# Performance work log

Measured on AMD Instinct MI355X. Metric: run time of the kernel, lower is better.

Reference implementation:

```python
import jax, jax.numpy as jnp
import numpy as np


def _inside_quad(pts9, quads):
    """Ray-casting point-in-polygon test (semantics of the pointsJf CUDA kernel),
    evaluated only for matched (diagonal) point/box pairs.

    pts9:  [N, 9, 2] points
    quads: [N, 8] polygon corners (x1,y1,x2,y2,x3,y3,x4,y4)
    returns inside flag [N, 9] float32 in {0.0, 1.0}
    """
    vx = quads[:, 0::2][:, None, :]          # [N,1,4]
    vy = quads[:, 1::2][:, None, :]          # [N,1,4]
    vxj = jnp.roll(vx, 1, axis=-1)           # previous vertex (j = i-1 mod 4)
    vyj = jnp.roll(vy, 1, axis=-1)
    px = pts9[..., 0:1]                      # [N,9,1]
    py = pts9[..., 1:2]                      # [N,9,1]
    straddles = (vy > py) != (vyj > py)      # edge crosses horizontal ray
    # x coordinate of edge at height py (only meaningful where straddles)
    x_int = (vxj - vx) * (py - vy) / (vyj - vy) + vx
    crossings = straddles & (px < x_int)     # [N,9,4] bool
    inside = (jnp.sum(crossings.astype(jnp.int32), axis=-1) % 2)
    return inside.astype(jnp.float32)        # [N,9]


def _spatial_border_loss(pts, gt_bboxes, weight, loss_weight):
    n = pts.shape[0]
    pts9 = pts.reshape(n, 9, 2)
    inside = _inside_quad(pts9, gt_bboxes)                    # [N,9]
    out_mask = (inside == 0.0).astype(pts.dtype)              # points outside their gt box
    cx = (gt_bboxes[:, 0] + gt_bboxes[:, 4]) * 0.5
    cy = (gt_bboxes[:, 1] + gt_bboxes[:, 5]) * 0.5
    center = jnp.stack([cx, cy], axis=1)[:, None, :]          # [N,1,2]
    dist = 0.2 * jnp.sqrt(jnp.sum((pts9 - center) ** 2, axis=-1))  # [N,9]
    cnt = jnp.sum(out_mask)
    loss_sb = jnp.where(cnt > 0, jnp.sum(dist * out_mask) / jnp.maximum(cnt, 1.0), 0.0)
    # weighted_spatial_border_loss: avg_factor = sum(weight_repeated4 > 0)/4 + 1e-6
    avg_factor = jnp.sum((weight > 0).astype(jnp.float32)) + 1e-6
    return loss_weight * (loss_sb / avg_factor)[None]          # shape [1]


def setup_inputs() -> dict:
    key = jax.random.key(0)
    k1, k2, k3 = jax.random.split(key, 3)
    N = 1_000_000
    pts = jax.random.normal(k1, (N, 18), dtype=jnp.float32)
    gt_bboxes = jax.random.normal(k2, (N, 8), dtype=jnp.float32)
    weight = jax.random.uniform(k3, (N,), dtype=jnp.float32)
    return {"pts": pts, "gt_bboxes": gt_bboxes, "weight": weight}


def reference(pts, gt_bboxes, weight):
    return _spatial_border_loss(pts, gt_bboxes, weight, loss_weight=1.0)
```

## Files before the change

kernel.cpp:

```cpp
#include <hip/hip_runtime.h>


#define SBL_NBLOCKS 2048
#define SBL_BLOCK   256

__global__ void __launch_bounds__(SBL_BLOCK) sbl_main(
    const float* __restrict__ pts,
    const float* __restrict__ quads,
    const float* __restrict__ weight,
    double* __restrict__ part_sum,
    unsigned int* __restrict__ part_cnt,
    unsigned int* __restrict__ part_wpos,
    int n)
{
    const int gid    = blockIdx.x * SBL_BLOCK + threadIdx.x;
    const int stride = gridDim.x * SBL_BLOCK;
    const int total  = n * 9;

    const float2* __restrict__ p2 = reinterpret_cast<const float2*>(pts);
    const float4* __restrict__ q4 = reinterpret_cast<const float4*>(quads);

    float local_sum = 0.0f;
    unsigned int local_cnt = 0u;
    unsigned int local_wpos = 0u;

    for (int p = gid; p < total; p += stride) {
        const int row = (int)((unsigned int)p / 9u);

        const float2 pxy = p2[p];
        const float px = pxy.x, py = pxy.y;

        const float4 qa = q4[(size_t)row * 2];
        const float4 qb = q4[(size_t)row * 2 + 1];
        const float vx0 = qa.x, vy0 = qa.y, vx1 = qa.z, vy1 = qa.w;
        const float vx2 = qb.x, vy2 = qb.y, vx3 = qb.z, vy3 = qb.w;

        int crossings = 0;
        #define SBL_EDGE(VX, VY, VXJ, VYJ)                                   \
        do {                                                                 \
            bool str_ = ((VY) > py) != ((VYJ) > py);                         \
            float d   = (VYJ) - (VY);                                        \
            float num = ((VXJ) - (VX)) * (py - (VY));                        \
            float lhs = (px - (VX)) * d;                                     \
            bool cond = (d > 0.0f) ? (lhs < num) : (lhs > num);              \
            crossings += (str_ && cond) ? 1 : 0;                             \
        } while (0)

        SBL_EDGE(vx0, vy0, vx3, vy3);
        SBL_EDGE(vx1, vy1, vx0, vy0);
        SBL_EDGE(vx2, vy2, vx1, vy1);
        SBL_EDGE(vx3, vy3, vx2, vy2);
        #undef SBL_EDGE

        if ((crossings & 1) == 0) {
            const float cx = (vx0 + vx2) * 0.5f;
            const float cy = (vy0 + vy2) * 0.5f;
            const float dx = px - cx;
            const float dy = py - cy;
            local_sum += 0.2f * sqrtf(dx * dx + dy * dy);
            local_cnt += 1u;
        }
    }

    for (int i = gid; i < n; i += stride) {
        local_wpos += (weight[i] > 0.0f) ? 1u : 0u;
    }

    #pragma unroll
    for (int off = 32; off > 0; off >>= 1) {
        local_sum  += __shfl_down(local_sum, off, 64);
        local_cnt  += __shfl_down(local_cnt, off, 64);
        local_wpos += __shfl_down(local_wpos, off, 64);
    }

    __shared__ float        s_sum[4];
    __shared__ unsigned int s_cnt[4];
    __shared__ unsigned int s_wpos[4];
    const int lane = threadIdx.x & 63;
    const int wave = threadIdx.x >> 6;
    if (lane == 0) { s_sum[wave] = local_sum; s_cnt[wave] = local_cnt; s_wpos[wave] = local_wpos; }
    __syncthreads();
    if (threadIdx.x == 0) {
        double bsum = 0.0;
        unsigned int bcnt = 0u, bwpos = 0u;
        #pragma unroll
        for (int i = 0; i < 4; ++i) { bsum += (double)s_sum[i]; bcnt += s_cnt[i]; bwpos += s_wpos[i]; }
        part_sum[blockIdx.x]  = bsum;
        part_cnt[blockIdx.x]  = bcnt;
        part_wpos[blockIdx.x] = bwpos;
    }
}

__global__ void __launch_bounds__(64) sbl_finalize(
    const double* __restrict__ part_sum,
    const unsigned int* __restrict__ part_cnt,
    const unsigned int* __restrict__ part_wpos,
    float* __restrict__ out,
    int nblocks)
{
    const int lane = threadIdx.x;
    double s = 0.0;
    unsigned int c = 0u, w = 0u;
    for (int i = lane; i < nblocks; i += 64) {
        s += part_sum[i];
        c += part_cnt[i];
        w += part_wpos[i];
    }
    #pragma unroll
    for (int off = 32; off > 0; off >>= 1) {
        s += __shfl_down(s, off, 64);
        c += __shfl_down(c, off, 64);
        w += __shfl_down(w, off, 64);
    }
    if (lane == 0) {
        double loss_sb = (c > 0u) ? (s / (double)c) : 0.0;
        double avg_factor = (double)w + 1e-6;
        out[0] = (float)(loss_sb / avg_factor);
    }
}

extern "C" void kernel_launch(void* const* d_in, const int* in_sizes, int n_in,
                              void* d_out, int out_size, void* d_ws, size_t ws_size,
                              hipStream_t stream) {
    const float* pts    = (const float*)d_in[0];
    const float* quads  = (const float*)d_in[1];
    const float* weight = (const float*)d_in[2];
    float* out = (float*)d_out;

    const int n = in_sizes[2];

    double*       part_sum  = (double*)d_ws;
    unsigned int* part_cnt  = (unsigned int*)((char*)d_ws + SBL_NBLOCKS * sizeof(double));
    unsigned int* part_wpos = (unsigned int*)((char*)d_ws + SBL_NBLOCKS * (sizeof(double) + sizeof(unsigned int)));

    sbl_main<<<SBL_NBLOCKS, SBL_BLOCK, 0, stream>>>(pts, quads, weight,
                                                    part_sum, part_cnt, part_wpos, n);
    sbl_finalize<<<1, 64, 0, stream>>>(part_sum, part_cnt, part_wpos, out, SBL_NBLOCKS);
}
```

Measured before the change: 142.5 us.

## Switch to one row per thread with LDS-staged point tiles

The grid-stride loop over individual points is replaced by one row per thread. Each block stages a 256-row tile of points into shared memory with coalesced float4 loads, loads each quad once per row instead of once per point, hoists the edge differences out of the nine-point loop, and computes parity with XORs. The 0.2 scale moves into the finalize step. The grid grows to about 3900 blocks, so the finalize kernel now reduces many more partials with 256 threads. Reading 18 floats per thread from LDS at that stride may cause bank conflicts.

```diff
diff --git a/kernel.cpp b/kernel.cpp
--- a/kernel.cpp
+++ b/kernel.cpp
@@ -1,8 +1,8 @@
 #include <hip/hip_runtime.h>
 
 
-#define SBL_NBLOCKS 2048
-#define SBL_BLOCK   256
+#define SBL_BLOCK 256
+#define SBL_TILE  256
 
 __global__ void __launch_bounds__(SBL_BLOCK) sbl_main(
     const float* __restrict__ pts,
@@ -13,57 +13,80 @@
     unsigned int* __restrict__ part_wpos,
     int n)
 {
-    const int gid    = blockIdx.x * SBL_BLOCK + threadIdx.x;
-    const int stride = gridDim.x * SBL_BLOCK;
-    const int total  = n * 9;
+    __shared__ float s_pts[SBL_TILE * 18];
 
-    const float2* __restrict__ p2 = reinterpret_cast<const float2*>(pts);
-    const float4* __restrict__ q4 = reinterpret_cast<const float4*>(quads);
+    const int tid  = threadIdx.x;
+    const int base = blockIdx.x * SBL_TILE;
+    const int rows = min(SBL_TILE, n - base);
+    const bool have_row = (tid < rows);
 
     float local_sum = 0.0f;
-    unsigned int local_cnt = 0u;
-    unsigned int local_wpos = 0u;
+    unsigned int local_cnt = 0u, local_wpos = 0u;
 
-    for (int p = gid; p < total; p += stride) {
-        const int row = (int)((unsigned int)p / 9u);
+    float4 qa = make_float4(0.f, 0.f, 0.f, 0.f);
+    float4 qb = make_float4(0.f, 0.f, 0.f, 0.f);
+    if (have_row) {
+        const float4* q4 = reinterpret_cast<const float4*>(quads) + (size_t)(base + tid) * 2;
+        qa = q4[0];
+        qb = q4[1];
+    }
+    {
+        const int gi = base + tid;
+        if (gi < n) local_wpos = (weight[gi] > 0.0f) ? 1u : 0u;
+    }
 
-        const float2 pxy = p2[p];
-        const float px = pxy.x, py = pxy.y;
+    if (rows == SBL_TILE) {
+        const float4* g4 = reinterpret_cast<const float4*>(pts + (size_t)base * 18);
+        float4* s4 = reinterpret_cast<float4*>(s_pts);
+        #pragma unroll
+        for (int k = 0; k < 5; ++k) {
+            const int idx = k * SBL_BLOCK + tid;
+            if (idx < (SBL_TILE * 18) / 4) s4[idx] = g4[idx];
+        }
+    } else {
+        const float2* g2 = reinterpret_cast<const float2*>(pts + (size_t)base * 18);
+        float2* s2 = reinterpret_cast<float2*>(s_pts);
+        const int nf2 = rows * 9;
+        for (int idx = tid; idx < nf2; idx += SBL_BLOCK) s2[idx] = g2[idx];
+    }
+    __syncthreads();
 
-        const float4 qa = q4[(size_t)row * 2];
-        const float4 qb = q4[(size_t)row * 2 + 1];
+    if (have_row) {
         const float vx0 = qa.x, vy0 = qa.y, vx1 = qa.z, vy1 = qa.w;
         const float vx2 = qb.x, vy2 = qb.y, vx3 = qb.z, vy3 = qb.w;
+        const float cx = (vx0 + vx2) * 0.5f;
+        const float cy = (vy0 + vy2) * 0.5f;
+        const float d0 = vy3 - vy0, d1 = vy0 - vy1, d2 = vy1 - vy2, d3 = vy2 - vy3;
+        const float e0 = vx3 - vx0, e1 = vx0 - vx1, e2 = vx1 - vx2, e3 = vx2 - vx3;
+        const bool  n0 = d0 < 0.0f, n1 = d1 < 0.0f, n2 = d2 < 0.0f, n3 = d3 < 0.0f;
 
-        int crossings = 0;
-        #define SBL_EDGE(VX, VY, VXJ, VYJ)                                   \
-        do {                                                                 \
-            bool str_ = ((VY) > py) != ((VYJ) > py);                         \
-            float d   = (VYJ) - (VY);                                        \
-            float num = ((VXJ) - (VX)) * (py - (VY));                        \
-            float lhs = (px - (VX)) * d;                                     \
-            bool cond = (d > 0.0f) ? (lhs < num) : (lhs > num);              \
-            crossings += (str_ && cond) ? 1 : 0;                             \
-        } while (0)
+        const float2* prow = reinterpret_cast<const float2*>(s_pts + tid * 18);
+        #pragma unroll
+        for (int k = 0; k < 9; ++k) {
+            const float2 p = prow[k];
+            const float px = p.x, py = p.y;
 
-        SBL_EDGE(vx0, vy0, vx3, vy3);
-        SBL_EDGE(vx1, vy1, vx0, vy0);
-        SBL_EDGE(vx2, vy2, vx1, vy1);
-        SBL_EDGE(vx3, vy3, vx2, vy2);
-        #undef SBL_EDGE
+            const bool c0 = vy0 > py, c1 = vy1 > py, c2 = vy2 > py, c3 = vy3 > py;
+            const bool s0 = c0 != c3, s1 = c1 != c0, s2 = c2 != c1, s3 = c3 != c2;
 
-        if ((crossings & 1) == 0) {
-            const float cx = (vx0 + vx2) * 0.5f;
-            const float cy = (vy0 + vy2) * 0.5f;
-            const float dx = px - cx;
-            const float dy = py - cy;
-            local_sum += 0.2f * sqrtf(dx * dx + dy * dy);
-            local_cnt += 1u;
+            const float t0 = py - vy0, t1 = py - vy1, t2 = py - vy2, t3 = py - vy3;
+            const float m0 = e0 * t0, m1 = e1 * t1, m2 = e2 * t2, m3 = e3 * t3;
+            const float l0 = (px - vx0) * d0, l1 = (px - vx1) * d1;
+            const float l2 = (px - vx2) * d2, l3 = (px - vx3) * d3;
+
+            const bool x0 = s0 && ((l0 < m0) != n0);
+            const bool x1 = s1 && ((l1 < m1) != n1);
+            const bool x2 = s2 && ((l2 < m2) != n2);
+            const bool x3 = s3 && ((l3 < m3) != n3);
+
+            const bool inside = (x0 != x1) != (x2 != x3);
+            if (!inside) {
+                const float dx = px - cx;
+                const float dy = py - cy;
+                local_sum += sqrtf(fmaf(dx, dx, dy * dy));
+                local_cnt += 1u;
+            }
         }
-    }
-
-    for (int i = gid; i < n; i += stride) {
-        local_wpos += (weight[i] > 0.0f) ? 1u : 0u;
     }
 
     #pragma unroll
@@ -73,35 +96,35 @@
         local_wpos += __shfl_down(local_wpos, off, 64);
     }
 
-    __shared__ float        s_sum[4];
-    __shared__ unsigned int s_cnt[4];
-    __shared__ unsigned int s_wpos[4];
-    const int lane = threadIdx.x & 63;
-    const int wave = threadIdx.x >> 6;
-    if (lane == 0) { s_sum[wave] = local_sum; s_cnt[wave] = local_cnt; s_wpos[wave] = local_wpos; }
+    __shared__ float        r_sum[4];
+    __shared__ unsigned int r_cnt[4];
+    __shared__ unsigned int r_wpos[4];
+    const int lane = tid & 63;
+    const int wave = tid >> 6;
+    if (lane == 0) { r_sum[wave] = local_sum; r_cnt[wave] = local_cnt; r_wpos[wave] = local_wpos; }
     __syncthreads();
-    if (threadIdx.x == 0) {
+    if (tid == 0) {
         double bsum = 0.0;
         unsigned int bcnt = 0u, bwpos = 0u;
         #pragma unroll
-        for (int i = 0; i < 4; ++i) { bsum += (double)s_sum[i]; bcnt += s_cnt[i]; bwpos += s_wpos[i]; }
+        for (int i = 0; i < 4; ++i) { bsum += (double)r_sum[i]; bcnt += r_cnt[i]; bwpos += r_wpos[i]; }
         part_sum[blockIdx.x]  = bsum;
         part_cnt[blockIdx.x]  = bcnt;
         part_wpos[blockIdx.x] = bwpos;
     }
 }
 
-__global__ void __launch_bounds__(64) sbl_finalize(
+__global__ void __launch_bounds__(256) sbl_finalize(
     const double* __restrict__ part_sum,
     const unsigned int* __restrict__ part_cnt,
     const unsigned int* __restrict__ part_wpos,
     float* __restrict__ out,
     int nblocks)
 {
-    const int lane = threadIdx.x;
+    const int tid = threadIdx.x;
     double s = 0.0;
     unsigned int c = 0u, w = 0u;
-    for (int i = lane; i < nblocks; i += 64) {
+    for (int i = tid; i < nblocks; i += 256) {
         s += part_sum[i];
         c += part_cnt[i];
         w += part_wpos[i];
@@ -112,9 +135,17 @@
         c += __shfl_down(c, off, 64);
         w += __shfl_down(w, off, 64);
     }
-    if (lane == 0) {
-        double loss_sb = (c > 0u) ? (s / (double)c) : 0.0;
-        double avg_factor = (double)w + 1e-6;
+    __shared__ double       fs[4];
+    __shared__ unsigned int fc[4], fw[4];
+    const int lane = tid & 63, wave = tid >> 6;
+    if (lane == 0) { fs[wave] = s; fc[wave] = c; fw[wave] = w; }
+    __syncthreads();
+    if (tid == 0) {
+        double ts = 0.0; unsigned int tc = 0u, tw = 0u;
+        #pragma unroll
+        for (int k = 0; k < 4; ++k) { ts += fs[k]; tc += fc[k]; tw += fw[k]; }
+        const double loss_sb = (tc > 0u) ? (0.2 * ts / (double)tc) : 0.0;
+        const double avg_factor = (double)tw + 1e-6;
         out[0] = (float)(loss_sb / avg_factor);
     }
 }
@@ -128,12 +159,13 @@
     float* out = (float*)d_out;
 
     const int n = in_sizes[2];
+    const int nblocks = (n + SBL_TILE - 1) / SBL_TILE;
 
     double*       part_sum  = (double*)d_ws;
-    unsigned int* part_cnt  = (unsigned int*)((char*)d_ws + SBL_NBLOCKS * sizeof(double));
-    unsigned int* part_wpos = (unsigned int*)((char*)d_ws + SBL_NBLOCKS * (sizeof(double) + sizeof(unsigned int)));
+    unsigned int* part_cnt  = (unsigned int*)((char*)d_ws + (size_t)nblocks * sizeof(double));
+    unsigned int* part_wpos = (unsigned int*)((char*)d_ws + (size_t)nblocks * (sizeof(double) + sizeof(unsigned int)));
 
-    sbl_main<<<SBL_NBLOCKS, SBL_BLOCK, 0, stream>>>(pts, quads, weight,
-                                                    part_sum, part_cnt, part_wpos, n);
-    sbl_finalize<<<1, 64, 0, stream>>>(part_sum, part_cnt, part_wpos, out, SBL_NBLOCKS);
+    sbl_main<<<nblocks, SBL_BLOCK, 0, stream>>>(pts, quads, weight,
+                                                part_sum, part_cnt, part_wpos, n);
+    sbl_finalize<<<1, 256, 0, stream>>>(part_sum, part_cnt, part_wpos, out, nblocks);
 }
```

Measured after the change: 140.8 us. Within noise of the previous version (-1.2%).
